# Performance work log

Hardware: AMD Instinct MI355X
Metric: run time of the kernel (lower is better)

The kernel has to match this reference:

```python
import jax, jax.numpy as jnp
import numpy as np
import math

B, S, HID, NH = 2, 1024, 4096, 32
HD = HID // NH  # 128


def setup_inputs() -> dict:
    key = jax.random.key(0)
    ks = jax.random.split(key, 6)
    scale = 0.02
    x = jax.random.normal(ks[0], (B, S, HID), dtype=jnp.float32)
    Wq = jax.random.normal(ks[1], (HID, HID), dtype=jnp.float32) * scale
    Wk = jax.random.normal(ks[2], (HID, HID), dtype=jnp.float32) * scale
    Wv = jax.random.normal(ks[3], (HID, HID), dtype=jnp.float32) * scale
    Wo = jax.random.normal(ks[4], (HID, HID), dtype=jnp.float32) * scale
    bq = jnp.zeros((HID,), jnp.float32)
    bk = jnp.zeros((HID,), jnp.float32)
    bv = jnp.zeros((HID,), jnp.float32)
    bo = jnp.zeros((HID,), jnp.float32)
    position_ids = jnp.tile(jnp.arange(S, dtype=jnp.int32)[None, :], (B, 1))
    # additive causal mask: 0 on/below diagonal, large negative above
    causal = jnp.tril(jnp.ones((S, S), dtype=bool))
    attention_mask = jnp.where(causal, 0.0, -1e9).astype(jnp.float32)[None, None]
    return {"x": x, "Wq": Wq, "bq": bq, "Wk": Wk, "bk": bk, "Wv": Wv,
            "bv": bv, "Wo": Wo, "bo": bo, "position_ids": position_ids,
            "attention_mask": attention_mask}


def _rotate_interleaved(t):
    # stack([-t[..., 1::2], t[..., ::2]], -1).reshape_as(t)
    return jnp.stack([-t[..., 1::2], t[..., ::2]], axis=-1).reshape(t.shape)


def reference(x, Wq, bq, Wk, bk, Wv, bv, Wo, bo, position_ids, attention_mask):
    b, s, _ = x.shape
    q = x @ Wq.T + bq
    k = x @ Wk.T + bk
    v = x @ Wv.T + bv
    # [B, NH, S, HD]
    q = q.reshape(b, s, NH, HD).transpose(0, 2, 1, 3)
    k = k.reshape(b, s, NH, HD).transpose(0, 2, 1, 3)
    v = v.reshape(b, s, NH, HD).transpose(0, 2, 1, 3)
    # RoPE (interleaved pairs), cos/sin recomputed each call as in source
    inv_freq = 1.0 / (10000.0 ** (jnp.arange(0, HD, 2, dtype=jnp.float32) / HD))
    ang = position_ids.astype(jnp.float32)[..., None] * inv_freq  # [B,S,HD/2]
    cos = jnp.repeat(jnp.cos(ang), 2, axis=-1)[:, None]  # [B,1,S,HD]
    sin = jnp.repeat(jnp.sin(ang), 2, axis=-1)[:, None]
    q = q * cos + _rotate_interleaved(q) * sin
    k = k * cos + _rotate_interleaved(k) * sin
    # naive full attention
    scores = jnp.einsum('bhqd,bhkd->bhqk', q, k) / math.sqrt(HD)
    scores = scores + attention_mask
    probs = jax.nn.softmax(scores, axis=-1)
    out = jnp.einsum('bhqk,bhkd->bhqd', probs, v)
    out = out.transpose(0, 2, 1, 3).reshape(b, s, HID)
    return out @ Wo.T + bo
```

## Files before the change

### kernel.cpp

```cpp
#include <hip/hip_runtime.h>
#include <hip/hip_bf16.h>
#include <cmath>

constexpr int cB  = 2;
constexpr int cS  = 1024;
constexpr int cNH = 32;
constexpr int cHD = 128;
constexpr int cHID = 4096;
constexpr int cM  = cB * cS;

typedef unsigned short u16;
typedef __bf16 bf16x8 __attribute__((ext_vector_type(8)));
typedef float  f32x4  __attribute__((ext_vector_type(4)));

__device__ __forceinline__ u16 f2b(float f) { return __builtin_bit_cast(u16, (__bf16)f); }

__global__ void cvt_bf16(const float* __restrict__ in, u16* __restrict__ out, int n8) {
  int i = blockIdx.x * blockDim.x + threadIdx.x;
  if (i >= n8) return;
  const float4* in4 = (const float4*)in;
  float4 a = in4[2 * i], b = in4[2 * i + 1];
  union { u16 u[8]; uint4 v; } r;
  r.u[0] = f2b(a.x); r.u[1] = f2b(a.y); r.u[2] = f2b(a.z); r.u[3] = f2b(a.w);
  r.u[4] = f2b(b.x); r.u[5] = f2b(b.y); r.u[6] = f2b(b.z); r.u[7] = f2b(b.w);
  ((uint4*)out)[i] = r.v;
}

__global__ void cvt3(const float* __restrict__ A0, const float* __restrict__ A1,
                     const float* __restrict__ A2,
                     u16* __restrict__ O0, u16* __restrict__ O1, u16* __restrict__ O2) {
  int idx = blockIdx.x * blockDim.x + threadIdx.x;
  int sel = idx >> 21, t = idx & ((1 << 21) - 1);
  const float* in = (sel == 0) ? A0 : (sel == 1 ? A1 : A2);
  u16* out = (sel == 0) ? O0 : (sel == 1 ? O1 : O2);
  const float4* in4 = (const float4*)in;
  float4 a = in4[2 * t], b = in4[2 * t + 1];
  union { u16 u[8]; uint4 v; } rv;
  rv.u[0] = f2b(a.x); rv.u[1] = f2b(a.y); rv.u[2] = f2b(a.z); rv.u[3] = f2b(a.w);
  rv.u[4] = f2b(b.x); rv.u[5] = f2b(b.y); rv.u[6] = f2b(b.z); rv.u[7] = f2b(b.w);
  ((uint4*)out)[t] = rv.v;
}

__global__ void rope_table_k(const int* __restrict__ pos,
                             float* __restrict__ cosT, float* __restrict__ sinT) {
  int idx = blockIdx.x * blockDim.x + threadIdx.x;
  int i = idx & 63, bs = idx >> 6;
  float p = (float)pos[bs];
  float freq = exp2f(-(float)i * (13.287712379549449f / 64.0f));
  float a = p * freq;
  float s, c;
  sincosf(a, &s, &c);
  cosT[idx] = c; sinT[idx] = s;
}

__global__ void rope_apply(u16* __restrict__ Q, u16* __restrict__ Kb,
                           const float* __restrict__ cosT, const float* __restrict__ sinT) {
  int idx = blockIdx.x * blockDim.x + threadIdx.x;
  const int nPer = cB * cS * cNH * (cHD / 8);
  u16* P = (idx < nPer) ? Q : Kb;
  int t = (idx < nPer) ? idx : idx - nPer;
  int d8 = t & 15;
  int h  = (t >> 4) & 31;
  int bs = t >> 9;
  size_t base = ((size_t)bs * cNH + h) * cHD + d8 * 8;
  uint4 v = *reinterpret_cast<uint4*>(P + base);
  u16* u = reinterpret_cast<u16*>(&v);
  int pb = bs * 64 + d8 * 4;
  float4 cs = *reinterpret_cast<const float4*>(cosT + pb);
  float4 sn = *reinterpret_cast<const float4*>(sinT + pb);
  float co[4] = {cs.x, cs.y, cs.z, cs.w};
  float si[4] = {sn.x, sn.y, sn.z, sn.w};
#pragma unroll
  for (int p = 0; p < 4; ++p) {
    float e = (float)__builtin_bit_cast(__bf16, u[2 * p]);
    float o = (float)__builtin_bit_cast(__bf16, u[2 * p + 1]);
    float e2 = e * co[p] - o * si[p];
    float o2 = o * co[p] + e * si[p];
    u[2 * p]     = f2b(e2);
    u[2 * p + 1] = f2b(o2);
  }
  *reinterpret_cast<uint4*>(P + base) = v;
}

__global__ void transpose_v(const u16* __restrict__ V, u16* __restrict__ Vt) {
  __shared__ u16 tile[32][33];
  int bh = blockIdx.z;
  int b = bh >> 5, h = bh & 31;
  int s0 = blockIdx.x * 32, d0 = blockIdx.y * 32;
  int tx = threadIdx.x & 31, ty0 = threadIdx.x >> 5;
#pragma unroll
  for (int i = 0; i < 4; ++i) {
    int r = ty0 + i * 8;
    tile[r][tx] = V[((size_t)(b * cS + s0 + r) * cNH + h) * cHD + d0 + tx];
  }
  __syncthreads();
#pragma unroll
  for (int i = 0; i < 4; ++i) {
    int r = ty0 + i * 8;
    Vt[((size_t)bh * cHD + d0 + r) * cS + s0 + tx] = tile[tx][r];
  }
}

template <int MODE>
__global__ __launch_bounds__(512, 2)
void gemm8(const u16* __restrict__ A,
           const u16* __restrict__ W0, const u16* __restrict__ W1,
           const u16* __restrict__ W2,
           const float* __restrict__ b0, const float* __restrict__ b1,
           const float* __restrict__ b2,
           void* o0, void* o1, void* o2) {
  __shared__ __align__(16) u16 sA[3][128 * 64];
  __shared__ __align__(16) u16 sB[3][256 * 64];
  const int tid = threadIdx.x;
  const int wid = tid >> 6, lane = tid & 63;
  const int c = lane & 15, g = lane >> 4;
  const int wm = wid >> 2, wn = wid & 3;
  const int m0 = blockIdx.x * 128;
  const int gn0 = blockIdx.y * 256;
  const int sel = gn0 >> 12;
  const int n0 = gn0 & 4095;
  const u16* Bw = (sel == 0) ? W0 : (sel == 1 ? W1 : W2);

  f32x4 acc[4][4] = {};
  const int nkt = cHID / 64;

#define STAGE_A(kt, dst)                                                       \
  {                                                                            \
    _Pragma("unroll") for (int l = 0; l < 2; ++l) {                            \
      int chunk = (l * 8 + wid) * 64 + lane;                                   \
      int row = chunk >> 3, kc = (chunk & 7) ^ (row & 7);                      \
      __builtin_amdgcn_global_load_lds(                                        \
          (const void*)(A + (size_t)(m0 + row) * cHID + (kt) * 64 + kc * 8),   \
          (void*)(&sA[dst][(l * 8 + wid) * 512]), 16, 0, 0);                   \
    }                                                                          \
  }
#define STAGE_B(kt, dst)                                                       \
  {                                                                            \
    _Pragma("unroll") for (int l = 0; l < 4; ++l) {                            \
      int chunk = (l * 8 + wid) * 64 + lane;                                   \
      int row = chunk >> 3, kc = (chunk & 7) ^ (row & 7);                      \
      __builtin_amdgcn_global_load_lds(                                        \
          (const void*)(Bw + (size_t)(n0 + row) * cHID + (kt) * 64 + kc * 8),  \
          (void*)(&sB[dst][(l * 8 + wid) * 512]), 16, 0, 0);                   \
    }                                                                          \
  }

  STAGE_A(0, 0); STAGE_B(0, 0);
  STAGE_A(1, 1); STAGE_B(1, 1);
  asm volatile("s_waitcnt vmcnt(6)" ::: "memory");
  __builtin_amdgcn_sched_barrier(0);
  __builtin_amdgcn_s_barrier();
  asm volatile("" ::: "memory");
  __builtin_amdgcn_sched_barrier(0);

  for (int kt = 0; kt < nkt; ++kt) {
    const int bufR = kt % 3;
    const int bufW = (kt + 2) % 3;
    const bool doStage = (kt + 2) < nkt;

    bf16x8 af[4], bw[4];
#pragma unroll
    for (int mf = 0; mf < 4; ++mf) {
      int ra = wm * 64 + mf * 16 + c;
      af[mf] = *reinterpret_cast<const bf16x8*>(
          &sA[bufR][ra * 64 + ((g ^ (ra & 7)) * 8)]);
    }
#pragma unroll
    for (int nf = 0; nf < 4; ++nf) {
      int rb = wn * 64 + nf * 16 + c;
      bw[nf] = *reinterpret_cast<const bf16x8*>(
          &sB[bufR][rb * 64 + ((g ^ (rb & 7)) * 8)]);
    }
    if (doStage) STAGE_A(kt + 2, bufW);
    __builtin_amdgcn_s_setprio(1);
#pragma unroll
    for (int mf = 0; mf < 4; ++mf)
#pragma unroll
      for (int nf = 0; nf < 4; ++nf)
        acc[mf][nf] = __builtin_amdgcn_mfma_f32_16x16x32_bf16(af[mf], bw[nf], acc[mf][nf], 0, 0, 0);
    __builtin_amdgcn_s_setprio(0);

#pragma unroll
    for (int mf = 0; mf < 4; ++mf) {
      int ra = wm * 64 + mf * 16 + c;
      af[mf] = *reinterpret_cast<const bf16x8*>(
          &sA[bufR][ra * 64 + (((4 + g) ^ (ra & 7)) * 8)]);
    }
#pragma unroll
    for (int nf = 0; nf < 4; ++nf) {
      int rb = wn * 64 + nf * 16 + c;
      bw[nf] = *reinterpret_cast<const bf16x8*>(
          &sB[bufR][rb * 64 + (((4 + g) ^ (rb & 7)) * 8)]);
    }
    if (doStage) STAGE_B(kt + 2, bufW);
    __builtin_amdgcn_s_setprio(1);
#pragma unroll
    for (int mf = 0; mf < 4; ++mf)
#pragma unroll
      for (int nf = 0; nf < 4; ++nf)
        acc[mf][nf] = __builtin_amdgcn_mfma_f32_16x16x32_bf16(af[mf], bw[nf], acc[mf][nf], 0, 0, 0);
    __builtin_amdgcn_s_setprio(0);

    if (doStage) {
      asm volatile("s_waitcnt vmcnt(6)" ::: "memory");
    } else {
      asm volatile("s_waitcnt vmcnt(0)" ::: "memory");
    }
    __builtin_amdgcn_sched_barrier(0);
    __builtin_amdgcn_s_barrier();
    asm volatile("" ::: "memory");
    __builtin_amdgcn_sched_barrier(0);
  }
#undef STAGE_A
#undef STAGE_B

  const float* bp = (sel == 0) ? b0 : (sel == 1 ? b1 : b2);
  void* op = (sel == 0) ? o0 : (sel == 1 ? o1 : o2);
#pragma unroll
  for (int nf = 0; nf < 4; ++nf) {
    int col = n0 + wn * 64 + nf * 16 + c;
    float bv = bp[col];
#pragma unroll
    for (int mf = 0; mf < 4; ++mf) {
      int row = m0 + wm * 64 + mf * 16 + g * 4;
#pragma unroll
      for (int r = 0; r < 4; ++r) {
        float v = acc[mf][nf][r] + bv;
        if (MODE == 0)
          ((u16*)op)[(size_t)(row + r) * cHID + col] = f2b(v);
        else
          ((float*)op)[(size_t)(row + r) * cHID + col] = v;
      }
    }
  }
}

__global__ __launch_bounds__(512, 4)
void attn_kernel(const u16* __restrict__ Q, const u16* __restrict__ Kb,
                 const u16* __restrict__ Vt, u16* __restrict__ O) {
  __shared__ __align__(16) char sK[2][16384];
  __shared__ __align__(16) char sP[16384];
  const int tid = threadIdx.x, wid = tid >> 6, lane = tid & 63;
  const int w = wid & 3, wg = wid >> 2;
  const int c = lane & 15, g = lane >> 4;
  const int bh = blockIdx.y;
  const int b = bh >> 5, h = bh & 31;
  const int NT = cS / 64;
  const int qtA = blockIdx.x, qtB = NT - 1 - blockIdx.x;
  const int qt_s = wg ? qtA : qtB;
  const int q0_s = qt_s * 64;
  const float kSc = 0.12751744f;
  const u16* Vg = Vt + (size_t)bh * (cHD * cS);

  bf16x8 qf[4];
  {
    size_t qrow = ((size_t)(b * cS + q0_s + w * 16 + c) * cNH + h) * cHD;
#pragma unroll
    for (int df = 0; df < 4; ++df)
      qf[df] = *reinterpret_cast<const bf16x8*>(Q + qrow + df * 32 + g * 8);
  }

  f32x4 o[8] = {};
  float mx[4] = {-1e30f, -1e30f, -1e30f, -1e30f};
  float ls[4] = {0.f, 0.f, 0.f, 0.f};

  uint4 kv[2];
#define LOADT(t)                                                               \
  {                                                                            \
    _Pragma("unroll") for (int i = 0; i < 2; ++i) {                            \
      int cidx = i * 512 + tid;                                                \
      int row = cidx >> 4, ch = cidx & 15;                                     \
      kv[i] = *reinterpret_cast<const uint4*>(                                 \
          Kb + ((size_t)(b * cS + (t) * 64 + row) * cNH + h) * cHD + ch * 8);  \
    }                                                                          \
  }
#define WRITET(buf)                                                            \
  {                                                                            \
    _Pragma("unroll") for (int i = 0; i < 2; ++i) {                            \
      int cidx = i * 512 + tid;                                                \
      int row = cidx >> 4, ch = cidx & 15;                                     \
      *reinterpret_cast<uint4*>(sK[buf] + row * 256 + ((ch ^ (row & 7)) * 16)) = kv[i]; \
    }                                                                          \
  }

  LOADT(0);
  WRITET(0);
  int cur = 0;

  for (int t = 0; t <= qtB; ++t) {
    __syncthreads();
    if (t < qtB) LOADT(t + 1);

    if (t <= qt_s) {
      f32x4 sc[4] = {};
#pragma unroll
      for (int df = 0; df < 4; ++df) {
        bf16x8 kb[4];
#pragma unroll
        for (int cf = 0; cf < 4; ++cf) {
          int kr = cf * 16 + c;
          kb[cf] = *reinterpret_cast<const bf16x8*>(sK[cur] + kr * 256 + (((df * 4 + g) ^ (kr & 7)) * 16));
        }
#pragma unroll
        for (int cf = 0; cf < 4; ++cf)
          sc[cf] = __builtin_amdgcn_mfma_f32_16x16x32_bf16(qf[df], kb[cf], sc[cf], 0, 0, 0);
      }

      if (t == qt_s) {
#pragma unroll
        for (int cf = 0; cf < 4; ++cf) {
          int kg = t * 64 + cf * 16 + c;
#pragma unroll
          for (int r = 0; r < 4; ++r) {
            int qg = q0_s + w * 16 + g * 4 + r;
            if (kg > qg) sc[cf][r] = -1e30f;
          }
        }
      }

      float alpha[4];
#pragma unroll
      for (int r = 0; r < 4; ++r) {
        float v = fmaxf(fmaxf(sc[0][r], sc[1][r]), fmaxf(sc[2][r], sc[3][r]));
        v = fmaxf(v, __shfl_xor(v, 1));
        v = fmaxf(v, __shfl_xor(v, 2));
        v = fmaxf(v, __shfl_xor(v, 4));
        v = fmaxf(v, __shfl_xor(v, 8));
        float mn = fmaxf(mx[r], v);
        alpha[r] = exp2f((mx[r] - mn) * kSc);
        mx[r] = mn;
      }
      float rs[4] = {0.f, 0.f, 0.f, 0.f};
#pragma unroll
      for (int cf = 0; cf < 4; ++cf)
#pragma unroll
        for (int r = 0; r < 4; ++r) {
          float p = exp2f((sc[cf][r] - mx[r]) * kSc);
          sc[cf][r] = p;
          rs[r] += p;
        }
#pragma unroll
      for (int r = 0; r < 4; ++r) {
        float v = rs[r];
        v += __shfl_xor(v, 1); v += __shfl_xor(v, 2);
        v += __shfl_xor(v, 4); v += __shfl_xor(v, 8);
        ls[r] = ls[r] * alpha[r] + v;
      }
#pragma unroll
      for (int nf = 0; nf < 8; ++nf)
#pragma unroll
        for (int r = 0; r < 4; ++r)
          o[nf][r] *= alpha[r];

      char* myP = sP + wid * 2048;
#pragma unroll
      for (int cf = 0; cf < 4; ++cf) {
        int kcol = cf * 16 + c;
        int chunk = kcol >> 3, within = kcol & 7;
#pragma unroll
        for (int r = 0; r < 4; ++r) {
          int qr = g * 4 + r;
          *reinterpret_cast<u16*>(myP + qr * 128 + ((chunk ^ (qr & 7)) * 16) + within * 2) =
              f2b(sc[cf][r]);
        }
      }
      bf16x8 pa[2];
#pragma unroll
      for (int kf = 0; kf < 2; ++kf)
        pa[kf] = *reinterpret_cast<const bf16x8*>(myP + c * 128 + (((kf * 4 + g) ^ (c & 7)) * 16));

#pragma unroll
      for (int kf = 0; kf < 2; ++kf) {
#pragma unroll
        for (int h2 = 0; h2 < 2; ++h2) {
          bf16x8 vb[4];
#pragma unroll
          for (int j = 0; j < 4; ++j)
            vb[j] = *reinterpret_cast<const bf16x8*>(
                Vg + (size_t)((h2 * 4 + j) * 16 + c) * cS + t * 64 + (kf * 4 + g) * 8);
#pragma unroll
          for (int j = 0; j < 4; ++j)
            o[h2 * 4 + j] = __builtin_amdgcn_mfma_f32_16x16x32_bf16(pa[kf], vb[j], o[h2 * 4 + j], 0, 0, 0);
        }
      }
    }

    if (t < qtB) { WRITET(cur ^ 1); cur ^= 1; }
  }

  __syncthreads();
#pragma unroll
  for (int nf = 0; nf < 8; ++nf) {
#pragma unroll
    for (int r = 0; r < 4; ++r) {
      float v = o[nf][r] / ls[r];
      int qr = w * 16 + g * 4 + r;
      *reinterpret_cast<u16*>(sK[wg] + qr * 256 + (nf * 16 + c) * 2) = f2b(v);
    }
  }
  __syncthreads();
#pragma unroll
  for (int s = 0; s < 2; ++s) {
    int q0 = (s ? qtA : qtB) * 64;
#pragma unroll
    for (int i = 0; i < 2; ++i) {
      int cidx = i * 512 + tid;
      int row = cidx >> 4, ch = cidx & 15;
      uint4 v = *reinterpret_cast<const uint4*>(sK[s] + row * 256 + ch * 16);
      *reinterpret_cast<uint4*>(O + ((size_t)(b * cS + q0 + row) * cNH + h) * cHD + ch * 8) = v;
    }
  }
#undef LOADT
#undef WRITET
}

extern "C" void kernel_launch(void* const* d_in, const int* in_sizes, int n_in,
                              void* d_out, int out_size, void* d_ws, size_t ws_size,
                              hipStream_t stream) {
  const float* x  = (const float*)d_in[0];
  const float* Wq = (const float*)d_in[1];
  const float* bq = (const float*)d_in[2];
  const float* Wk = (const float*)d_in[3];
  const float* bk = (const float*)d_in[4];
  const float* Wv = (const float*)d_in[5];
  const float* bv = (const float*)d_in[6];
  const float* Wo = (const float*)d_in[7];
  const float* bo = (const float*)d_in[8];
  const int*  pos = (const int*)d_in[9];
  float* out = (float*)d_out;

  char* ws = (char*)d_ws;
  const size_t MB = 1u << 20;
  const int W8 = (cHID * cHID) / 8;
  const int X8 = (cM * cHID) / 8;
  const int R8 = cB * cS * cNH * (cHD / 8);

  if (ws_size >= 168 * MB) {
    u16* xb  = (u16*)(ws);
    u16* Qb  = (u16*)(ws + 16 * MB);
    u16* Kb  = (u16*)(ws + 32 * MB);
    u16* Vb  = (u16*)(ws + 48 * MB);
    float* cosT = (float*)(ws + 64 * MB);
    float* sinT = cosT + cB * cS * 64;
    u16* WbQ = (u16*)(ws + 72 * MB);
    u16* WbK = (u16*)(ws + 104 * MB);
    u16* WbV = (u16*)(ws + 136 * MB);
    u16* Vt  = WbQ;
    u16* Ab  = WbK;
    u16* WbO = WbV;

    cvt3<<<(3 * W8) / 256, 256, 0, stream>>>(Wq, Wk, Wv, WbQ, WbK, WbV);
    rope_table_k<<<(cB * cS * 64) / 256, 256, 0, stream>>>(pos, cosT, sinT);
    cvt_bf16<<<X8 / 256, 256, 0, stream>>>(x, xb, X8);

    gemm8<0><<<dim3(16, 48), 512, 0, stream>>>(
        xb, WbQ, WbK, WbV, bq, bk, bv, Qb, Kb, Vb);

    rope_apply<<<(2 * R8) / 256, 256, 0, stream>>>(Qb, Kb, cosT, sinT);
    transpose_v<<<dim3(cS / 32, cHD / 32, cB * cNH), 256, 0, stream>>>(Vb, Vt);
    attn_kernel<<<dim3(cS / 128, cB * cNH), 512, 0, stream>>>(Qb, Kb, Vt, Ab);

    cvt_bf16<<<W8 / 256, 256, 0, stream>>>(Wo, WbO, W8);
    gemm8<1><<<dim3(16, 16), 512, 0, stream>>>(
        Ab, WbO, WbO, WbO, bo, bo, bo, out, out, out);
  } else {
    u16* xb = (u16*)(ws);
    u16* Wb = (u16*)(ws + 16 * MB);
    u16* Qb = (u16*)(ws + 48 * MB);
    u16* Kb = (u16*)(ws + 64 * MB);
    u16* Vb = (u16*)(ws + 80 * MB);
    u16* Vt = xb;
    u16* Ab = Vb;
    float* cosT = (float*)(ws + 96 * MB);
    float* sinT = cosT + cB * cS * 64;

    cvt_bf16<<<X8 / 256, 256, 0, stream>>>(x, xb, X8);
    cvt_bf16<<<W8 / 256, 256, 0, stream>>>(Wq, Wb, W8);
    gemm8<0><<<dim3(16, 16), 512, 0, stream>>>(
        xb, Wb, Wb, Wb, bq, bq, bq, Qb, Qb, Qb);
    cvt_bf16<<<W8 / 256, 256, 0, stream>>>(Wk, Wb, W8);
    gemm8<0><<<dim3(16, 16), 512, 0, stream>>>(
        xb, Wb, Wb, Wb, bk, bk, bk, Kb, Kb, Kb);
    cvt_bf16<<<W8 / 256, 256, 0, stream>>>(Wv, Wb, W8);
    gemm8<0><<<dim3(16, 16), 512, 0, stream>>>(
        xb, Wb, Wb, Wb, bv, bv, bv, Vb, Vb, Vb);

    rope_table_k<<<(cB * cS * 64) / 256, 256, 0, stream>>>(pos, cosT, sinT);
    rope_apply<<<(2 * R8) / 256, 256, 0, stream>>>(Qb, Kb, cosT, sinT);
    transpose_v<<<dim3(cS / 32, cHD / 32, cB * cNH), 256, 0, stream>>>(Vb, Vt);
    attn_kernel<<<dim3(cS / 128, cB * cNH), 512, 0, stream>>>(Qb, Kb, Vt, Ab);

    cvt_bf16<<<W8 / 256, 256, 0, stream>>>(Wo, Wb, W8);
    gemm8<1><<<dim3(16, 16), 512, 0, stream>>>(
        Ab, Wb, Wb, Wb, bo, bo, bo, out, out, out);
  }
}
```

Baseline: 495.3 us.

## Split paired-tile attention blocks into one 64-row query tile per block

The attention kernel previously paired a short and a long causal query tile in one 512-thread block so both halves shared K tiles and the block's work stayed balanced. It now launches one 256-thread block per 64-row query tile, which doubles the grid and halves the per-block LDS for P. This drops the idle-wave branching and raises the number of blocks available for scheduling. In exchange, each K tile is loaded separately by more blocks, and block durations vary widely across the causal diagonal, so load balance depends on the hardware scheduler.

```diff
diff --git a/kernel.cpp b/kernel.cpp
--- a/kernel.cpp
+++ b/kernel.cpp
@@ -235,26 +235,24 @@
   }
 }
 
-__global__ __launch_bounds__(512, 4)
+__global__ __launch_bounds__(256, 4)
 void attn_kernel(const u16* __restrict__ Q, const u16* __restrict__ Kb,
                  const u16* __restrict__ Vt, u16* __restrict__ O) {
   __shared__ __align__(16) char sK[2][16384];
-  __shared__ __align__(16) char sP[16384];
-  const int tid = threadIdx.x, wid = tid >> 6, lane = tid & 63;
-  const int w = wid & 3, wg = wid >> 2;
+  __shared__ __align__(16) char sP[8192];
+  const int tid = threadIdx.x, w = tid >> 6, lane = tid & 63;
   const int c = lane & 15, g = lane >> 4;
   const int bh = blockIdx.y;
   const int b = bh >> 5, h = bh & 31;
   const int NT = cS / 64;
-  const int qtA = blockIdx.x, qtB = NT - 1 - blockIdx.x;
-  const int qt_s = wg ? qtA : qtB;
-  const int q0_s = qt_s * 64;
+  const int qt = NT - 1 - blockIdx.x;
+  const int q0 = qt * 64;
   const float kSc = 0.12751744f;
   const u16* Vg = Vt + (size_t)bh * (cHD * cS);
 
   bf16x8 qf[4];
   {
-    size_t qrow = ((size_t)(b * cS + q0_s + w * 16 + c) * cNH + h) * cHD;
+    size_t qrow = ((size_t)(b * cS + q0 + w * 16 + c) * cNH + h) * cHD;
 #pragma unroll
     for (int df = 0; df < 4; ++df)
       qf[df] = *reinterpret_cast<const bf16x8*>(Q + qrow + df * 32 + g * 8);
@@ -264,11 +262,11 @@
   float mx[4] = {-1e30f, -1e30f, -1e30f, -1e30f};
   float ls[4] = {0.f, 0.f, 0.f, 0.f};
 
-  uint4 kv[2];
+  uint4 kv[4];
 #define LOADT(t)                                                               \
   {                                                                            \
-    _Pragma("unroll") for (int i = 0; i < 2; ++i) {                            \
-      int cidx = i * 512 + tid;                                                \
+    _Pragma("unroll") for (int i = 0; i < 4; ++i) {                            \
+      int cidx = i * 256 + tid;                                                \
       int row = cidx >> 4, ch = cidx & 15;                                     \
       kv[i] = *reinterpret_cast<const uint4*>(                                 \
           Kb + ((size_t)(b * cS + (t) * 64 + row) * cNH + h) * cHD + ch * 8);  \
@@ -276,8 +274,8 @@
   }
 #define WRITET(buf)                                                            \
   {                                                                            \
-    _Pragma("unroll") for (int i = 0; i < 2; ++i) {                            \
-      int cidx = i * 512 + tid;                                                \
+    _Pragma("unroll") for (int i = 0; i < 4; ++i) {                            \
+      int cidx = i * 256 + tid;                                                \
       int row = cidx >> 4, ch = cidx & 15;                                     \
       *reinterpret_cast<uint4*>(sK[buf] + row * 256 + ((ch ^ (row & 7)) * 16)) = kv[i]; \
     }                                                                          \
@@ -287,105 +285,103 @@
   WRITET(0);
   int cur = 0;
 
-  for (int t = 0; t <= qtB; ++t) {
+  for (int t = 0; t <= qt; ++t) {
     __syncthreads();
-    if (t < qtB) LOADT(t + 1);
-
-    if (t <= qt_s) {
-      f32x4 sc[4] = {};
-#pragma unroll
-      for (int df = 0; df < 4; ++df) {
-        bf16x8 kb[4];
-#pragma unroll
-        for (int cf = 0; cf < 4; ++cf) {
-          int kr = cf * 16 + c;
-          kb[cf] = *reinterpret_cast<const bf16x8*>(sK[cur] + kr * 256 + (((df * 4 + g) ^ (kr & 7)) * 16));
+    if (t < qt) LOADT(t + 1);
+
+    f32x4 sc[4] = {};
+#pragma unroll
+    for (int df = 0; df < 4; ++df) {
+      bf16x8 kb[4];
+#pragma unroll
+      for (int cf = 0; cf < 4; ++cf) {
+        int kr = cf * 16 + c;
+        kb[cf] = *reinterpret_cast<const bf16x8*>(sK[cur] + kr * 256 + (((df * 4 + g) ^ (kr & 7)) * 16));
+      }
+#pragma unroll
+      for (int cf = 0; cf < 4; ++cf)
+        sc[cf] = __builtin_amdgcn_mfma_f32_16x16x32_bf16(qf[df], kb[cf], sc[cf], 0, 0, 0);
+    }
+
+    if (t == qt) {
+#pragma unroll
+      for (int cf = 0; cf < 4; ++cf) {
+        int kg = t * 64 + cf * 16 + c;
+#pragma unroll
+        for (int r = 0; r < 4; ++r) {
+          int qg = q0 + w * 16 + g * 4 + r;
+          if (kg > qg) sc[cf][r] = -1e30f;
         }
-#pragma unroll
-        for (int cf = 0; cf < 4; ++cf)
-          sc[cf] = __builtin_amdgcn_mfma_f32_16x16x32_bf16(qf[df], kb[cf], sc[cf], 0, 0, 0);
-      }
-
-      if (t == qt_s) {
-#pragma unroll
-        for (int cf = 0; cf < 4; ++cf) {
-          int kg = t * 64 + cf * 16 + c;
-#pragma unroll
-          for (int r = 0; r < 4; ++r) {
-            int qg = q0_s + w * 16 + g * 4 + r;
-            if (kg > qg) sc[cf][r] = -1e30f;
-          }
-        }
-      }
-
-      float alpha[4];
+      }
+    }
+
+    float alpha[4];
+#pragma unroll
+    for (int r = 0; r < 4; ++r) {
+      float v = fmaxf(fmaxf(sc[0][r], sc[1][r]), fmaxf(sc[2][r], sc[3][r]));
+      v = fmaxf(v, __shfl_xor(v, 1));
+      v = fmaxf(v, __shfl_xor(v, 2));
+      v = fmaxf(v, __shfl_xor(v, 4));
+      v = fmaxf(v, __shfl_xor(v, 8));
+      float mn = fmaxf(mx[r], v);
+      alpha[r] = exp2f((mx[r] - mn) * kSc);
+      mx[r] = mn;
+    }
+    float rs[4] = {0.f, 0.f, 0.f, 0.f};
+#pragma unroll
+    for (int cf = 0; cf < 4; ++cf)
 #pragma unroll
       for (int r = 0; r < 4; ++r) {
-        float v = fmaxf(fmaxf(sc[0][r], sc[1][r]), fmaxf(sc[2][r], sc[3][r]));
-        v = fmaxf(v, __shfl_xor(v, 1));
-        v = fmaxf(v, __shfl_xor(v, 2));
-        v = fmaxf(v, __shfl_xor(v, 4));
-        v = fmaxf(v, __shfl_xor(v, 8));
-        float mn = fmaxf(mx[r], v);
-        alpha[r] = exp2f((mx[r] - mn) * kSc);
-        mx[r] = mn;
-      }
-      float rs[4] = {0.f, 0.f, 0.f, 0.f};
-#pragma unroll
-      for (int cf = 0; cf < 4; ++cf)
-#pragma unroll
-        for (int r = 0; r < 4; ++r) {
-          float p = exp2f((sc[cf][r] - mx[r]) * kSc);
-          sc[cf][r] = p;
-          rs[r] += p;
-        }
+        float p = exp2f((sc[cf][r] - mx[r]) * kSc);
+        sc[cf][r] = p;
+        rs[r] += p;
+      }
+#pragma unroll
+    for (int r = 0; r < 4; ++r) {
+      float v = rs[r];
+      v += __shfl_xor(v, 1); v += __shfl_xor(v, 2);
+      v += __shfl_xor(v, 4); v += __shfl_xor(v, 8);
+      ls[r] = ls[r] * alpha[r] + v;
+    }
+#pragma unroll
+    for (int nf = 0; nf < 8; ++nf)
+#pragma unroll
+      for (int r = 0; r < 4; ++r)
+        o[nf][r] *= alpha[r];
+
+    char* myP = sP + w * 2048;
+#pragma unroll
+    for (int cf = 0; cf < 4; ++cf) {
+      int kcol = cf * 16 + c;
+      int chunk = kcol >> 3, within = kcol & 7;
 #pragma unroll
       for (int r = 0; r < 4; ++r) {
-        float v = rs[r];
-        v += __shfl_xor(v, 1); v += __shfl_xor(v, 2);
-        v += __shfl_xor(v, 4); v += __shfl_xor(v, 8);
-        ls[r] = ls[r] * alpha[r] + v;
-      }
-#pragma unroll
-      for (int nf = 0; nf < 8; ++nf)
-#pragma unroll
-        for (int r = 0; r < 4; ++r)
-          o[nf][r] *= alpha[r];
-
-      char* myP = sP + wid * 2048;
-#pragma unroll
-      for (int cf = 0; cf < 4; ++cf) {
-        int kcol = cf * 16 + c;
-        int chunk = kcol >> 3, within = kcol & 7;
-#pragma unroll
-        for (int r = 0; r < 4; ++r) {
-          int qr = g * 4 + r;
-          *reinterpret_cast<u16*>(myP + qr * 128 + ((chunk ^ (qr & 7)) * 16) + within * 2) =
-              f2b(sc[cf][r]);
-        }
-      }
-      bf16x8 pa[2];
-#pragma unroll
-      for (int kf = 0; kf < 2; ++kf)
-        pa[kf] = *reinterpret_cast<const bf16x8*>(myP + c * 128 + (((kf * 4 + g) ^ (c & 7)) * 16));
-
-#pragma unroll
-      for (int kf = 0; kf < 2; ++kf) {
-#pragma unroll
-        for (int h2 = 0; h2 < 2; ++h2) {
-          bf16x8 vb[4];
-#pragma unroll
-          for (int j = 0; j < 4; ++j)
-            vb[j] = *reinterpret_cast<const bf16x8*>(
-                Vg + (size_t)((h2 * 4 + j) * 16 + c) * cS + t * 64 + (kf * 4 + g) * 8);
-#pragma unroll
-          for (int j = 0; j < 4; ++j)
-            o[h2 * 4 + j] = __builtin_amdgcn_mfma_f32_16x16x32_bf16(pa[kf], vb[j], o[h2 * 4 + j], 0, 0, 0);
-        }
-      }
-    }
-
-    if (t < qtB) { WRITET(cur ^ 1); cur ^= 1; }
+        int qr = g * 4 + r;
+        *reinterpret_cast<u16*>(myP + qr * 128 + ((chunk ^ (qr & 7)) * 16) + within * 2) =
+            f2b(sc[cf][r]);
+      }
+    }
+    bf16x8 pa[2];
+#pragma unroll
+    for (int kf = 0; kf < 2; ++kf)
+      pa[kf] = *reinterpret_cast<const bf16x8*>(myP + c * 128 + (((kf * 4 + g) ^ (c & 7)) * 16));
+
+#pragma unroll
+    for (int kf = 0; kf < 2; ++kf) {
+#pragma unroll
+      for (int h2 = 0; h2 < 2; ++h2) {
+        bf16x8 vb[4];
+#pragma unroll
+        for (int j = 0; j < 4; ++j)
+          vb[j] = *reinterpret_cast<const bf16x8*>(
+              Vg + (size_t)((h2 * 4 + j) * 16 + c) * cS + t * 64 + (kf * 4 + g) * 8);
+#pragma unroll
+        for (int j = 0; j < 4; ++j)
+          o[h2 * 4 + j] = __builtin_amdgcn_mfma_f32_16x16x32_bf16(pa[kf], vb[j], o[h2 * 4 + j], 0, 0, 0);
+      }
+    }
+
+    if (t < qt) { WRITET(cur ^ 1); cur ^= 1; }
   }
 
   __syncthreads();
@@ -395,20 +391,16 @@
     for (int r = 0; r < 4; ++r) {
       float v = o[nf][r] / ls[r];
       int qr = w * 16 + g * 4 + r;
-      *reinterpret_cast<u16*>(sK[wg] + qr * 256 + (nf * 16 + c) * 2) = f2b(v);
+      *reinterpret_cast<u16*>(sK[0] + qr * 256 + (nf * 16 + c) * 2) = f2b(v);
     }
   }
   __syncthreads();
 #pragma unroll
-  for (int s = 0; s < 2; ++s) {
-    int q0 = (s ? qtA : qtB) * 64;
-#pragma unroll
-    for (int i = 0; i < 2; ++i) {
-      int cidx = i * 512 + tid;
-      int row = cidx >> 4, ch = cidx & 15;
-      uint4 v = *reinterpret_cast<const uint4*>(sK[s] + row * 256 + ch * 16);
-      *reinterpret_cast<uint4*>(O + ((size_t)(b * cS + q0 + row) * cNH + h) * cHD + ch * 8) = v;
-    }
+  for (int i = 0; i < 4; ++i) {
+    int cidx = i * 256 + tid;
+    int row = cidx >> 4, ch = cidx & 15;
+    uint4 v = *reinterpret_cast<const uint4*>(sK[0] + row * 256 + ch * 16);
+    *reinterpret_cast<uint4*>(O + ((size_t)(b * cS + q0 + row) * cNH + h) * cHD + ch * 8) = v;
   }
 #undef LOADT
 #undef WRITET
@@ -458,7 +450,7 @@
 
     rope_apply<<<(2 * R8) / 256, 256, 0, stream>>>(Qb, Kb, cosT, sinT);
     transpose_v<<<dim3(cS / 32, cHD / 32, cB * cNH), 256, 0, stream>>>(Vb, Vt);
-    attn_kernel<<<dim3(cS / 128, cB * cNH), 512, 0, stream>>>(Qb, Kb, Vt, Ab);
+    attn_kernel<<<dim3(cS / 64, cB * cNH), 256, 0, stream>>>(Qb, Kb, Vt, Ab);
 
     cvt_bf16<<<W8 / 256, 256, 0, stream>>>(Wo, WbO, W8);
     gemm8<1><<<dim3(16, 16), 512, 0, stream>>>(
@@ -488,7 +480,7 @@
     rope_table_k<<<(cB * cS * 64) / 256, 256, 0, stream>>>(pos, cosT, sinT);
     rope_apply<<<(2 * R8) / 256, 256, 0, stream>>>(Qb, Kb, cosT, sinT);
     transpose_v<<<dim3(cS / 32, cHD / 32, cB * cNH), 256, 0, stream>>>(Vb, Vt);
-    attn_kernel<<<dim3(cS / 128, cB * cNH), 512, 0, stream>>>(Qb, Kb, Vt, Ab);
+    attn_kernel<<<dim3(cS / 64, cB * cNH), 256, 0, stream>>>(Qb, Kb, Vt, Ab);
 
     cvt_bf16<<<W8 / 256, 256, 0, stream>>>(Wo, Wb, W8);
     gemm8<1><<<dim3(16, 16), 512, 0, stream>>>(
```

After: 645.8 us. +30.4%, slower.
